# Kernel tuning notes

Hardware: AMD Instinct MI355X
Metric: run time of the kernel (lower is better)

## Reference

```python
import jax, jax.numpy as jnp
import numpy as np

B, T, C = 4, 2048, 1024
H = 16
HD = C // H


def setup_inputs() -> dict:
    key = jax.random.key(0)
    k1, k2, k3 = jax.random.split(key, 3)
    x = jax.random.normal(k1, (B, T, C), dtype=jnp.float32)
    w_qkv = jax.random.normal(k2, (C, 3 * C), dtype=jnp.float32) * (C ** -0.5)
    w_proj = jax.random.normal(k3, (C, C), dtype=jnp.float32) * (C ** -0.5)
    b_proj = jnp.zeros((C,), dtype=jnp.float32)
    return {"x": x, "w_qkv": w_qkv, "w_proj": w_proj, "b_proj": b_proj}


def reference(x, w_qkv, w_proj, b_proj):
    Bd, Td, Cd = x.shape
    scale = HD ** -0.5
    qkv = x @ w_qkv  # [B,T,3C]
    q, k, v = jnp.split(qkv, 3, axis=-1)
    # [B,H,T,HD]
    q = q.reshape(Bd, Td, H, HD).transpose(0, 2, 1, 3)
    k = k.reshape(Bd, Td, H, HD).transpose(0, 2, 1, 3)
    v = v.reshape(Bd, Td, H, HD).transpose(0, 2, 1, 3)
    att = jnp.einsum('bhqd,bhkd->bhqk', q, k) * scale
    causal = jnp.triu(jnp.ones((Td, Td), dtype=bool), k=1)
    att = jnp.where(causal, -jnp.inf, att)
    att = jax.nn.softmax(att, axis=-1)
    y = jnp.einsum('bhqk,bhkd->bhqd', att, v)
    y = y.transpose(0, 2, 1, 3).reshape(Bd, Td, Cd)
    return y @ w_proj + b_proj
```

## Files before the change

### kernel.cpp

```cpp
#include <hip/hip_runtime.h>

typedef unsigned short u16;
typedef __attribute__((ext_vector_type(8))) short short8;
typedef __attribute__((ext_vector_type(4))) short short4v;
typedef __attribute__((ext_vector_type(4))) float floatx4;
typedef __attribute__((ext_vector_type(4))) unsigned short ushort4v;

#define B_ 4
#define T_ 2048
#define C_ 1024
#define H_ 16
#define HD_ 64

static __device__ __forceinline__ u16 f2bf(float f) {
  union { float f; unsigned int i; } c; c.f = f;
  unsigned int u = c.i;
  return (u16)((u + 0x7FFFu + ((u >> 16) & 1u)) >> 16);
}
static __device__ __forceinline__ unsigned pk2(float lo, float hi) {
  union { float f; unsigned u; } a, b; a.f = hi; b.f = lo;
  return __builtin_amdgcn_perm(a.u, b.u, 0x07060302u);
}
static __device__ __forceinline__ unsigned pk2r(float lo, float hi) {
  return (unsigned)f2bf(lo) | ((unsigned)f2bf(hi) << 16);
}

static __device__ __forceinline__ void gload16(const u16* g, u16* l) {
  __builtin_amdgcn_global_load_lds(
      (const __attribute__((address_space(1))) unsigned int*)(g),
      (__attribute__((address_space(3))) unsigned int*)(l), 16, 0, 0);
}

__global__ __launch_bounds__(256) void prep_k(const float* __restrict__ x,
                                              const float* __restrict__ w_qkv,
                                              const float* __restrict__ w_proj,
                                              u16* __restrict__ xbf,
                                              u16* __restrict__ wqkvT,
                                              u16* __restrict__ wprojT) {
  const int bid = blockIdx.x;
  if (bid < 8192) {
    const int i = bid * 256 + threadIdx.x;
    const float4 f = ((const float4*)x)[i];
    ushort4v o;
    o.x = f2bf(f.x); o.y = f2bf(f.y); o.z = f2bf(f.z); o.w = f2bf(f.w);
    *(ushort4v*)(xbf + (size_t)i * 4) = o;
    return;
  }
  __shared__ u16 tile[32][33];
  const float* in;
  u16* out;
  int R, Cc, tb;
  if (bid < 11264) {
    in = w_qkv; out = wqkvT; R = C_; Cc = 3 * C_; tb = bid - 8192;
  } else {
    in = w_proj; out = wprojT; R = C_; Cc = C_; tb = bid - 11264;
  }
  const int tpr = Cc / 32;
  const int bx = (tb % tpr) * 32;
  const int by = (tb / tpr) * 32;
  const int tx = threadIdx.x & 31;
  const int ty = threadIdx.x >> 5;
  #pragma unroll
  for (int i = ty; i < 32; i += 8)
    tile[i][tx] = f2bf(in[(size_t)(by + i) * Cc + bx + tx]);
  __syncthreads();
  #pragma unroll
  for (int i = ty; i < 32; i += 8)
    out[(size_t)(bx + i) * R + by + tx] = tile[tx][i];
}

template <int MODE>
__global__ __launch_bounds__(256) void gemm_bt(const u16* __restrict__ A,
                                               const u16* __restrict__ Bt,
                                               u16* __restrict__ outb,
                                               u16* __restrict__ outv,
                                               float* __restrict__ outf,
                                               const float* __restrict__ bias,
                                               int M, int N, int K) {
  __shared__ __align__(16) u16 lds[16384];
  const int bid = blockIdx.x;
  const int s = bid >> 3;
  const int tM = ((bid & 7) * 8 + (s & 7)) * 128;
  const int tN = (s >> 3) * 128;
  const int tid = threadIdx.x;
  const int wave = tid >> 6;
  const int lane = tid & 63;
  const int lr = lane & 15;
  const int quad = lane >> 4;
  const int wm = (wave >> 1) * 64;
  const int wn = (wave & 1) * 64;

  const int srow = lane >> 2;
  const int skofs = ((lane & 3) ^ ((lane >> 3) & 3)) * 8;

  const floatx4 zf = {0.f, 0.f, 0.f, 0.f};
  floatx4 acc[4][4];
  #pragma unroll
  for (int i = 0; i < 4; i++)
    #pragma unroll
    for (int j = 0; j < 4; j++) acc[i][j] = zf;

  const int csw = (lr >> 1) & 3;

  for (int k0 = 0; k0 < K; k0 += 64) {
    __syncthreads();
    #pragma unroll
    for (int half = 0; half < 2; half++) {
      const int kk = k0 + half * 32;
      #pragma unroll
      for (int j = 0; j < 2; j++) {
        const int seg = wave * 2 + j;
        const int row = seg * 16 + srow;
        gload16(A + (size_t)(tM + row) * K + kk + skofs, &lds[half * 4096 + seg * 512]);
        gload16(Bt + (size_t)(tN + row) * K + kk + skofs, &lds[8192 + half * 4096 + seg * 512]);
      }
    }
    __syncthreads();

    #pragma unroll
    for (int half = 0; half < 2; half++) {
      short8 af[4], bfr[4];
      #pragma unroll
      for (int mt = 0; mt < 4; mt++)
        af[mt] = *(const short8*)(&lds[half * 4096 + (wm + mt * 16 + lr) * 32 + ((quad ^ csw) * 8)]);
      #pragma unroll
      for (int nt = 0; nt < 4; nt++)
        bfr[nt] = *(const short8*)(&lds[8192 + half * 4096 + (wn + nt * 16 + lr) * 32 + ((quad ^ csw) * 8)]);
      #pragma unroll
      for (int mt = 0; mt < 4; mt++)
        #pragma unroll
        for (int nt = 0; nt < 4; nt++)
          acc[mt][nt] = __builtin_amdgcn_mfma_f32_16x16x32_bf16(af[mt], bfr[nt],
                                                                acc[mt][nt], 0, 0, 0);
    }
  }

  if (MODE == 1 && tN >= 2 * C_) {
    const int b = tM >> 11;
    const int t0 = tM & (T_ - 1);
    const int h0 = (tN - 2 * C_) >> 6;
    #pragma unroll
    for (int pass = 0; pass < 2; pass++) {
      __syncthreads();
      if ((wave & 1) == pass) {
        #pragma unroll
        for (int nt = 0; nt < 4; nt++) {
          const int nr = nt * 16 + lr;
          #pragma unroll
          for (int mt = 0; mt < 4; mt++) {
            const int mr = wm + mt * 16 + quad * 4;
            *(unsigned*)(&lds[nr * 136 + mr]) = pk2r(acc[mt][nt][0], acc[mt][nt][1]);
            *(unsigned*)(&lds[nr * 136 + mr + 2]) = pk2r(acc[mt][nt][2], acc[mt][nt][3]);
          }
        }
      }
      __syncthreads();
      const int bh = b * H_ + h0 + pass;
      u16* vbase = outv + (size_t)bh * HD_ * T_ + t0;
      #pragma unroll
      for (int i = 0; i < 4; i++) {
        const int c = tid + i * 256;
        const int nr = c >> 4, m8 = (c & 15) * 8;
        const short8 v = *(const short8*)(&lds[nr * 136 + m8]);
        *(short8*)(vbase + (size_t)nr * T_ + m8) = v;
      }
    }
    return;
  }

  #pragma unroll
  for (int mt = 0; mt < 4; mt++) {
    const int m0 = tM + wm + mt * 16 + quad * 4;
    #pragma unroll
    for (int nt = 0; nt < 4; nt++) {
      const int n = tN + wn + nt * 16 + lr;
      #pragma unroll
      for (int r = 0; r < 4; r++) {
        const float v = acc[mt][nt][r];
        const size_t m = (size_t)(m0 + r);
        if (MODE == 2) __builtin_nontemporal_store(v + bias[n], &outf[m * N + n]);
        else           outb[m * N + n] = f2bf(v);
      }
    }
  }
}

__global__ __launch_bounds__(256, 4) void attn_k(const u16* __restrict__ qkv,
                                                 const u16* __restrict__ vt,
                                                 u16* __restrict__ y) {
  __shared__ __align__(16) u16 Ks[64 * 64];
  __shared__ __align__(16) u16 Vs[64 * 64];
  const int bid = blockIdx.x;
  const int s = bid >> 3;
  const int qp = s >> 3;
  const int bh = ((s & 7) << 3) | (bid & 7);
  const int b = bh >> 4, h = bh & 15;
  const int tid = threadIdx.x;
  const int wave = tid >> 6;
  const int lane = tid & 63;
  const int lr = lane & 15;
  const int quad = lane >> 4;
  const int qtA = qp, qtB = 31 - qp;

  const int srow = lane >> 3;
  const int skofs = ((lane & 7) ^ ((lane >> 3) & 7)) * 8;
  const int gsw = lr & 7;

  const size_t RS = 3 * C_;
  const u16* qcol = qkv + (size_t)b * T_ * RS + h * HD_;
  const u16* kcol = qcol + C_;

  const size_t qrA = (size_t)(qtA * 64 + wave * 16 + lr) * RS;
  const size_t qrB = (size_t)(qtB * 64 + wave * 16 + lr) * RS;
  const short8 aq0A = *(const short8*)(qcol + qrA + quad * 8);
  const short8 aq1A = *(const short8*)(qcol + qrA + 32 + quad * 8);
  const short8 aq0B = *(const short8*)(qcol + qrB + quad * 8);
  const short8 aq1B = *(const short8*)(qcol + qrB + 32 + quad * 8);

  const floatx4 zf = {0.f, 0.f, 0.f, 0.f};
  const float C1 = 0.125f * 1.44269504f;
  const float C2 = -16.0f * 1.44269504f;
  const short8 vones = {16256, 16256, 16256, 16256, 16256, 16256, 16256, 16256};

  floatx4 accA[4], accB[4];
  floatx4 accSA = zf, accSB = zf;
  #pragma unroll
  for (int i = 0; i < 4; i++) { accA[i] = zf; accB[i] = zf; }

  for (int kt = 0; kt <= qtB; kt++) {
    const bool doA = (kt <= qtA);
    const bool diagA = (kt == qtA), diagB = (kt == qtB);
    __syncthreads();
    #pragma unroll
    for (int j = 0; j < 2; j++) {
      const int seg = wave * 2 + j;
      const int row = seg * 8 + srow;
      gload16(kcol + (size_t)(kt * 64 + row) * RS + skofs, &Ks[seg * 512]);
      gload16(vt + ((size_t)bh * HD_ + row) * T_ + kt * 64 + skofs, &Vs[seg * 512]);
    }
    __syncthreads();

    float peA[4][4], peB[4][4];
    #pragma unroll
    for (int nt = 0; nt < 4; nt++) {
      const short8 bk0 =
          *(const short8*)(&Ks[(nt * 16 + lr) * 64 + ((quad ^ gsw) * 8)]);
      const short8 bk1 =
          *(const short8*)(&Ks[(nt * 16 + lr) * 64 + (((quad + 4) ^ gsw) * 8)]);
      {
        floatx4 st = __builtin_amdgcn_mfma_f32_16x16x32_bf16(
            bk1, aq1B,
            __builtin_amdgcn_mfma_f32_16x16x32_bf16(bk0, aq0B, zf, 0, 0, 0),
            0, 0, 0);
        #pragma unroll
        for (int r = 0; r < 4; r++) {
          float pe = __builtin_amdgcn_exp2f(fmaf(st[r], C1, C2));
          if (diagB && (nt * 16 + quad * 4 + r > wave * 16 + lr)) pe = 0.f;
          peB[nt][r] = pe;
        }
      }
      if (doA) {
        floatx4 st = __builtin_amdgcn_mfma_f32_16x16x32_bf16(
            bk1, aq1A,
            __builtin_amdgcn_mfma_f32_16x16x32_bf16(bk0, aq0A, zf, 0, 0, 0),
            0, 0, 0);
        #pragma unroll
        for (int r = 0; r < 4; r++) {
          float pe = __builtin_amdgcn_exp2f(fmaf(st[r], C1, C2));
          if (diagA && (nt * 16 + quad * 4 + r > wave * 16 + lr)) pe = 0.f;
          peA[nt][r] = pe;
        }
      }
    }

    short8 pB[2], pA[2];
    #pragma unroll
    for (int h2 = 0; h2 < 2; h2++) {
      union { unsigned u[4]; short8 s8; } w;
      w.u[0] = pk2(peB[2 * h2][0], peB[2 * h2][1]);
      w.u[1] = pk2(peB[2 * h2][2], peB[2 * h2][3]);
      w.u[2] = pk2(peB[2 * h2 + 1][0], peB[2 * h2 + 1][1]);
      w.u[3] = pk2(peB[2 * h2 + 1][2], peB[2 * h2 + 1][3]);
      pB[h2] = w.s8;
    }
    if (doA) {
      #pragma unroll
      for (int h2 = 0; h2 < 2; h2++) {
        union { unsigned u[4]; short8 s8; } w;
        w.u[0] = pk2(peA[2 * h2][0], peA[2 * h2][1]);
        w.u[1] = pk2(peA[2 * h2][2], peA[2 * h2][3]);
        w.u[2] = pk2(peA[2 * h2 + 1][0], peA[2 * h2 + 1][1]);
        w.u[3] = pk2(peA[2 * h2 + 1][2], peA[2 * h2 + 1][3]);
        pA[h2] = w.s8;
      }
    }

    #pragma unroll
    for (int h2 = 0; h2 < 2; h2++) {
      accSB = __builtin_amdgcn_mfma_f32_16x16x32_bf16(vones, pB[h2], accSB, 0, 0, 0);
      if (doA)
        accSA = __builtin_amdgcn_mfma_f32_16x16x32_bf16(vones, pA[h2], accSA, 0, 0, 0);
      #pragma unroll
      for (int dt = 0; dt < 4; dt++) {
        const int base = (dt * 16 + lr) * 64;
        const int cl = h2 * 4 + (quad >> 1);
        const int off_lo = ((cl ^ gsw) * 8) + (quad & 1) * 4;
        const int off_hi = (((cl + 2) ^ gsw) * 8) + (quad & 1) * 4;
        const short4v vlo = *(const short4v*)(&Vs[base + off_lo]);
        const short4v vhi = *(const short4v*)(&Vs[base + off_hi]);
        const short8 av = __builtin_shufflevector(vlo, vhi, 0, 1, 2, 3, 4, 5, 6, 7);
        accB[dt] = __builtin_amdgcn_mfma_f32_16x16x32_bf16(av, pB[h2], accB[dt], 0, 0, 0);
        if (doA)
          accA[dt] = __builtin_amdgcn_mfma_f32_16x16x32_bf16(av, pA[h2], accA[dt], 0, 0, 0);
      }
    }
  }

  #pragma unroll
  for (int ph = 0; ph < 2; ph++) {
    const int qt = ph ? qtB : qtA;
    const floatx4* acc = ph ? accB : accA;
    const float inv = 1.f / (ph ? accSB[0] : accSA[0]);
    const int qg = qt * 64 + wave * 16 + lr;
    u16* yrow = y + ((size_t)(b * T_ + qg)) * C_ + h * HD_;
    #pragma unroll
    for (int dt = 0; dt < 4; dt++) {
      ushort4v o;
      #pragma unroll
      for (int r = 0; r < 4; r++) o[r] = f2bf(acc[dt][r] * inv);
      *(ushort4v*)(yrow + dt * 16 + quad * 4) = o;
    }
  }
}

extern "C" void kernel_launch(void* const* d_in, const int* in_sizes, int n_in,
                              void* d_out, int out_size, void* d_ws, size_t ws_size,
                              hipStream_t stream) {
  const float* x      = (const float*)d_in[0];
  const float* w_qkv  = (const float*)d_in[1];
  const float* w_proj = (const float*)d_in[2];
  const float* b_proj = (const float*)d_in[3];
  float* out = (float*)d_out;

  u16* ws = (u16*)d_ws;
  const size_t SZ = (size_t)B_ * T_ * C_;
  u16* xbf    = ws;
  u16* wqkvT  = xbf + SZ;
  u16* wprojT = wqkvT + (size_t)3 * C_ * C_;
  u16* qkvw   = wprojT + (size_t)C_ * C_;
  u16* vtw    = qkvw + 3 * SZ;
  u16* yw     = xbf;

  prep_k<<<12288, 256, 0, stream>>>(x, w_qkv, w_proj, xbf, wqkvT, wprojT);
  gemm_bt<1><<<1536, 256, 0, stream>>>(
      xbf, wqkvT, qkvw, vtw, nullptr, nullptr, B_ * T_, 3 * C_, C_);
  attn_k<<<1024, 256, 0, stream>>>(qkvw, vtw, yw);
  gemm_bt<2><<<512, 256, 0, stream>>>(
      yw, wprojT, nullptr, nullptr, out, b_proj, B_ * T_, C_, C_);
}
```

Measured before the change: 240.2 us.

## Specialize attention loop phases at compile time and halve output-projection N tile

The attention key-tile loop is split into four phases (both queries, diagonal A, B only, diagonal B), using compile-time flags. This removes the per-iteration branches on doA and the diagonal masks, so the common case runs without mask compares. The output-projection GEMM is templated on N-tile width and launched with 128x64 tiles over twice as many blocks, giving better occupancy and wave balance on the 512-block launch. The cost is larger code, more A-tile reloads, and lower arithmetic intensity per block in the projection GEMM.

```diff
diff --git a/kernel.cpp b/kernel.cpp
--- a/kernel.cpp
+++ b/kernel.cpp
@@ -11,6 +11,8 @@
 #define C_ 1024
 #define H_ 16
 #define HD_ 64
+
+template <bool V> struct BC { static constexpr bool value = V; };
 
 static __device__ __forceinline__ u16 f2bf(float f) {
   union { float f; unsigned int i; } c; c.f = f;
@@ -69,7 +71,7 @@
     out[(size_t)(bx + i) * R + by + tx] = tile[tx][i];
 }
 
-template <int MODE>
+template <int MODE, int NT>
 __global__ __launch_bounds__(256) void gemm_bt(const u16* __restrict__ A,
                                                const u16* __restrict__ Bt,
                                                u16* __restrict__ outb,
@@ -77,28 +79,28 @@
                                                float* __restrict__ outf,
                                                const float* __restrict__ bias,
                                                int M, int N, int K) {
-  __shared__ __align__(16) u16 lds[16384];
+  __shared__ __align__(16) u16 lds[8192 + NT * 2048];
   const int bid = blockIdx.x;
   const int s = bid >> 3;
   const int tM = ((bid & 7) * 8 + (s & 7)) * 128;
-  const int tN = (s >> 3) * 128;
+  const int tN = (s >> 3) * (NT * 32);
   const int tid = threadIdx.x;
   const int wave = tid >> 6;
   const int lane = tid & 63;
   const int lr = lane & 15;
   const int quad = lane >> 4;
   const int wm = (wave >> 1) * 64;
-  const int wn = (wave & 1) * 64;
+  const int wn = (wave & 1) * (NT * 16);
 
   const int srow = lane >> 2;
   const int skofs = ((lane & 3) ^ ((lane >> 3) & 3)) * 8;
 
   const floatx4 zf = {0.f, 0.f, 0.f, 0.f};
-  floatx4 acc[4][4];
+  floatx4 acc[4][NT];
   #pragma unroll
   for (int i = 0; i < 4; i++)
     #pragma unroll
-    for (int j = 0; j < 4; j++) acc[i][j] = zf;
+    for (int j = 0; j < NT; j++) acc[i][j] = zf;
 
   const int csw = (lr >> 1) & 3;
 
@@ -112,24 +114,30 @@
         const int seg = wave * 2 + j;
         const int row = seg * 16 + srow;
         gload16(A + (size_t)(tM + row) * K + kk + skofs, &lds[half * 4096 + seg * 512]);
-        gload16(Bt + (size_t)(tN + row) * K + kk + skofs, &lds[8192 + half * 4096 + seg * 512]);
+      }
+      #pragma unroll
+      for (int j = 0; j < NT / 2; j++) {
+        const int seg = wave * (NT / 2) + j;
+        const int row = seg * 16 + srow;
+        gload16(Bt + (size_t)(tN + row) * K + kk + skofs,
+                &lds[8192 + half * (NT * 1024) + seg * 512]);
       }
     }
     __syncthreads();
 
     #pragma unroll
     for (int half = 0; half < 2; half++) {
-      short8 af[4], bfr[4];
+      short8 af[4], bfr[NT];
       #pragma unroll
       for (int mt = 0; mt < 4; mt++)
         af[mt] = *(const short8*)(&lds[half * 4096 + (wm + mt * 16 + lr) * 32 + ((quad ^ csw) * 8)]);
       #pragma unroll
-      for (int nt = 0; nt < 4; nt++)
-        bfr[nt] = *(const short8*)(&lds[8192 + half * 4096 + (wn + nt * 16 + lr) * 32 + ((quad ^ csw) * 8)]);
+      for (int nt = 0; nt < NT; nt++)
+        bfr[nt] = *(const short8*)(&lds[8192 + half * (NT * 1024) + (wn + nt * 16 + lr) * 32 + ((quad ^ csw) * 8)]);
       #pragma unroll
       for (int mt = 0; mt < 4; mt++)
         #pragma unroll
-        for (int nt = 0; nt < 4; nt++)
+        for (int nt = 0; nt < NT; nt++)
           acc[mt][nt] = __builtin_amdgcn_mfma_f32_16x16x32_bf16(af[mt], bfr[nt],
                                                                 acc[mt][nt], 0, 0, 0);
     }
@@ -144,7 +152,7 @@
       __syncthreads();
       if ((wave & 1) == pass) {
         #pragma unroll
-        for (int nt = 0; nt < 4; nt++) {
+        for (int nt = 0; nt < NT; nt++) {
           const int nr = nt * 16 + lr;
           #pragma unroll
           for (int mt = 0; mt < 4; mt++) {
@@ -172,7 +180,7 @@
   for (int mt = 0; mt < 4; mt++) {
     const int m0 = tM + wm + mt * 16 + quad * 4;
     #pragma unroll
-    for (int nt = 0; nt < 4; nt++) {
+    for (int nt = 0; nt < NT; nt++) {
       const int n = tN + wn + nt * 16 + lr;
       #pragma unroll
       for (int r = 0; r < 4; r++) {
@@ -227,9 +235,7 @@
   #pragma unroll
   for (int i = 0; i < 4; i++) { accA[i] = zf; accB[i] = zf; }
 
-  for (int kt = 0; kt <= qtB; kt++) {
-    const bool doA = (kt <= qtA);
-    const bool diagA = (kt == qtA), diagB = (kt == qtB);
+  auto stage = [&](int kt) {
     __syncthreads();
     #pragma unroll
     for (int j = 0; j < 2; j++) {
@@ -239,7 +245,12 @@
       gload16(vt + ((size_t)bh * HD_ + row) * T_ + kt * 64 + skofs, &Vs[seg * 512]);
     }
     __syncthreads();
-
+  };
+
+  auto core = [&](auto WA, auto DA, auto DB) {
+    constexpr bool wA = decltype(WA)::value;
+    constexpr bool dA = decltype(DA)::value;
+    constexpr bool dB = decltype(DB)::value;
     float peA[4][4], peB[4][4];
     #pragma unroll
     for (int nt = 0; nt < 4; nt++) {
@@ -255,11 +266,12 @@
         #pragma unroll
         for (int r = 0; r < 4; r++) {
           float pe = __builtin_amdgcn_exp2f(fmaf(st[r], C1, C2));
-          if (diagB && (nt * 16 + quad * 4 + r > wave * 16 + lr)) pe = 0.f;
+          if constexpr (dB)
+            if (nt * 16 + quad * 4 + r > wave * 16 + lr) pe = 0.f;
           peB[nt][r] = pe;
         }
       }
-      if (doA) {
+      if constexpr (wA) {
         floatx4 st = __builtin_amdgcn_mfma_f32_16x16x32_bf16(
             bk1, aq1A,
             __builtin_amdgcn_mfma_f32_16x16x32_bf16(bk0, aq0A, zf, 0, 0, 0),
@@ -267,7 +279,8 @@
         #pragma unroll
         for (int r = 0; r < 4; r++) {
           float pe = __builtin_amdgcn_exp2f(fmaf(st[r], C1, C2));
-          if (diagA && (nt * 16 + quad * 4 + r > wave * 16 + lr)) pe = 0.f;
+          if constexpr (dA)
+            if (nt * 16 + quad * 4 + r > wave * 16 + lr) pe = 0.f;
           peA[nt][r] = pe;
         }
       }
@@ -283,7 +296,7 @@
       w.u[3] = pk2(peB[2 * h2 + 1][2], peB[2 * h2 + 1][3]);
       pB[h2] = w.s8;
     }
-    if (doA) {
+    if constexpr (wA) {
       #pragma unroll
       for (int h2 = 0; h2 < 2; h2++) {
         union { unsigned u[4]; short8 s8; } w;
@@ -298,7 +311,7 @@
     #pragma unroll
     for (int h2 = 0; h2 < 2; h2++) {
       accSB = __builtin_amdgcn_mfma_f32_16x16x32_bf16(vones, pB[h2], accSB, 0, 0, 0);
-      if (doA)
+      if constexpr (wA)
         accSA = __builtin_amdgcn_mfma_f32_16x16x32_bf16(vones, pA[h2], accSA, 0, 0, 0);
       #pragma unroll
       for (int dt = 0; dt < 4; dt++) {
@@ -310,11 +323,16 @@
         const short4v vhi = *(const short4v*)(&Vs[base + off_hi]);
         const short8 av = __builtin_shufflevector(vlo, vhi, 0, 1, 2, 3, 4, 5, 6, 7);
         accB[dt] = __builtin_amdgcn_mfma_f32_16x16x32_bf16(av, pB[h2], accB[dt], 0, 0, 0);
-        if (doA)
+        if constexpr (wA)
           accA[dt] = __builtin_amdgcn_mfma_f32_16x16x32_bf16(av, pA[h2], accA[dt], 0, 0, 0);
       }
     }
-  }
+  };
+
+  for (int kt = 0; kt < qtA; kt++) { stage(kt); core(BC<true>{}, BC<false>{}, BC<false>{}); }
+  stage(qtA); core(BC<true>{}, BC<true>{}, BC<false>{});
+  for (int kt = qtA + 1; kt < qtB; kt++) { stage(kt); core(BC<false>{}, BC<false>{}, BC<false>{}); }
+  stage(qtB); core(BC<false>{}, BC<false>{}, BC<true>{});
 
   #pragma unroll
   for (int ph = 0; ph < 2; ph++) {
@@ -352,9 +370,9 @@
   u16* yw     = xbf;
 
   prep_k<<<12288, 256, 0, stream>>>(x, w_qkv, w_proj, xbf, wqkvT, wprojT);
-  gemm_bt<1><<<1536, 256, 0, stream>>>(
+  gemm_bt<1, 4><<<1536, 256, 0, stream>>>(
       xbf, wqkvT, qkvw, vtw, nullptr, nullptr, B_ * T_, 3 * C_, C_);
   attn_k<<<1024, 256, 0, stream>>>(qkvw, vtw, yw);
-  gemm_bt<2><<<512, 256, 0, stream>>>(
+  gemm_bt<2, 2><<<1024, 256, 0, stream>>>(
       yw, wprojT, nullptr, nullptr, out, b_proj, B_ * T_, C_, C_);
 }
```

New measurement: 236.8 us. No clear change (-1.4%).
